# Performance work log

Measured on AMD Instinct MI355X. Metric: run time of the kernel, lower is better.

Reference implementation:

```python
import jax, jax.numpy as jnp
import numpy as np

R, H, K, C = 8, 8, 4096, 128  # residual stages, subvectors, codebook size, subvector dim
B, S = 2, 2048


def setup_inputs() -> dict:
    key = jax.random.key(0)
    k1, k2 = jax.random.split(key)
    x = jax.random.normal(k1, (B, S, H * C), dtype=jnp.float32)
    codebook = jax.random.normal(k2, (R, H, K, C), dtype=jnp.float32) * 0.1
    return {"x": x, "codebook": codebook}


def _encode(x, codebook):
    b, s, f = x.shape
    # x.view(b,s,8,2,64).transpose(3,4).flatten(2)  -> interleave the two 64-dim halves per head
    xp = x.reshape(b, s, 8, 2, 64).transpose(0, 1, 2, 4, 3).reshape(b, s, f)
    prescale = jnp.linalg.norm(xp, axis=-1, keepdims=True)  # (b,s,1)
    xn = xp / prescale
    # (b s) h c  -> permute to (h, N, c)
    t0 = xn.reshape(b * s, H, C).transpose(1, 0, 2)  # (H, N, C)

    def step(t, cb_r):
        # cb_r: (H, K, C). Squared-euclidean argmin == torch.cdist argmin (sqrt is monotone,
        # and the ||t||^2 term is constant over k so it is dropped).
        d = jnp.sum(cb_r * cb_r, axis=-1)[:, None, :] - 2.0 * jnp.einsum('hnc,hkc->hnk', t, cb_r)
        idx = jnp.argmin(d, axis=-1)  # (H, N)
        q = jnp.take_along_axis(cb_r, idx[..., None], axis=1)  # (H, N, C)
        return t - q, idx.astype(jnp.int32)

    _, codes = jax.lax.scan(step, t0, codebook)  # codes: (R, H, N)
    return codes, prescale


def _decode(codes, prescale, codebook):
    # gather codebook entries: (R, H, N, C)
    g = jnp.take_along_axis(codebook, codes[..., None], axis=2)
    n = codes.shape[2]
    # permute(0,2,1,3).flatten(-2).sum(0): (R,N,H*C) summed over residual stages
    rec = g.transpose(0, 2, 1, 3).reshape(R, n, H * C).sum(0)  # (N, H*C)
    b = prescale.shape[0]
    return rec.reshape(b, -1, H * C) * prescale


def reference(x, codebook):
    codes, prescale = _encode(x, codebook)
    return _decode(codes, prescale, codebook)
```

## Files before the change

### kernel.cpp

```cpp
#include <hip/hip_runtime.h>

#define R_STAGES 8
#define H_HEADS  8
#define K_CODES  4096
#define C_DIM    128
#define N_TOK    4096
#define FEAT     1024
#define HKC      (H_HEADS * K_CODES * C_DIM)

#define MARGIN   1.2e-2f
#define WCAP     512
#define TMS      260

typedef _Float16 half8  __attribute__((ext_vector_type(8)));
typedef _Float16 half4v __attribute__((ext_vector_type(4)));
typedef float    f32x4  __attribute__((ext_vector_type(4)));

#define MFMA16(A, B, C) __builtin_amdgcn_mfma_f32_16x16x32_f16((A), (B), (C), 0, 0, 0)


__global__ void kc_prep(const float* __restrict__ x, float* __restrict__ t,
                        float* __restrict__ ps) {
    int n = blockIdx.x;
    const float* xr = x + (size_t)n * FEAT;

    double ss = 0.0;
    for (int i = threadIdx.x; i < FEAT; i += 256) {
        float v = xr[i];
        ss += (double)v * (double)v;
    }
    for (int off = 32; off > 0; off >>= 1) ss += __shfl_down(ss, off);

    __shared__ double sred[4];
    __shared__ float s_p;
    int wid = threadIdx.x >> 6, lane = threadIdx.x & 63;
    if (lane == 0) sred[wid] = ss;
    __syncthreads();
    if (threadIdx.x == 0) {
        double tot = sred[0] + sred[1] + sred[2] + sred[3];
        float p = (float)sqrt(tot);
        ps[n] = p;
        s_p = p;
    }
    __syncthreads();
    float p = s_p;

    for (int i = threadIdx.x; i < FEAT; i += 256) {
        int c = i & 127;
        float v = xr[(i & ~127) + ((c & 1) << 6) + (c >> 1)];
        size_t o = ((size_t)(i >> 7) * N_TOK + n) * C_DIM + c;
        t[o] = v / p;
    }
}

__global__ void kc_cvtn(const float* __restrict__ cb, _Float16* __restrict__ cb16,
                        float* __restrict__ cn) {
    int w = (blockIdx.x << 2) + (threadIdx.x >> 6);
    int lane = threadIdx.x & 63;
    const float* row = cb + (size_t)w * C_DIM;
    float a = row[lane], b = row[lane + 64];
    _Float16* dr = cb16 + (size_t)w * C_DIM;
    dr[lane]      = (_Float16)a;
    dr[lane + 64] = (_Float16)b;
    double s = (double)a * a + (double)b * b;
    for (int off = 32; off > 0; off >>= 1) s += __shfl_down(s, off);
    if (lane == 0) cn[w] = (float)s;
}

__device__ __forceinline__ void stage_body(
    const float* __restrict__ cbh32, const _Float16* __restrict__ cbh16,
    const float* __restrict__ cnh, float* __restrict__ th) {

    __shared__ _Float16 tmin[64 * TMS];
    __shared__ float    rbs[256][4];
    __shared__ float    mtok[64];
    __shared__ int      wl[WCAP];
    __shared__ double   eD[WCAP];
    __shared__ int      eI[WCAP];
    __shared__ int      winner[64];
    __shared__ int      wlCnt;

    const int tid  = threadIdx.x;
    const int w    = tid >> 6;
    const int lane = tid & 63;
    const int col  = lane & 15;
    const int rblk = lane >> 4;

    if (tid == 0) wlCnt = 0;

    half8 tf[4][4];
#pragma unroll
    for (int g = 0; g < 4; ++g) {
        const float* trow = th + (size_t)(g * 16 + col) * C_DIM;
#pragma unroll
        for (int j = 0; j < 4; ++j) {
            const float* p = trow + j * 32 + rblk * 8;
            f32x4 lo = *(const f32x4*)p;
            f32x4 hi = *(const f32x4*)(p + 4);
            half8 v;
            v[0] = (_Float16)lo[0]; v[1] = (_Float16)lo[1];
            v[2] = (_Float16)lo[2]; v[3] = (_Float16)lo[3];
            v[4] = (_Float16)hi[0]; v[5] = (_Float16)hi[1];
            v[6] = (_Float16)hi[2]; v[7] = (_Float16)hi[3];
            tf[g][j] = v;
        }
    }

    const int kbase = w << 10;
    const _Float16* cbA = cbh16 + (size_t)(kbase + col) * C_DIM + rblk * 8;
    const float*    cnA = cnh + kbase + (rblk << 2);

    auto loadA = [&](int it, half8* A, f32x4& cv) {
        const _Float16* p = cbA + (size_t)it * (16 * C_DIM);
#pragma unroll
        for (int j = 0; j < 4; ++j) A[j] = *(const half8*)(p + j * 32);
        cv = *(const f32x4*)(cnA + it * 16);
    };

    float rbg0 = 3.4e38f, rbg1 = 3.4e38f, rbg2 = 3.4e38f, rbg3 = 3.4e38f;

    auto screen = [&](const half8* A, const f32x4& cv, int wtile) {
        f32x4 a0 = {0.f,0.f,0.f,0.f}, a1 = {0.f,0.f,0.f,0.f};
        f32x4 a2 = {0.f,0.f,0.f,0.f}, a3 = {0.f,0.f,0.f,0.f};
#pragma unroll
        for (int j = 0; j < 4; ++j) {
            a0 = MFMA16(A[j], tf[0][j], a0);
            a1 = MFMA16(A[j], tf[1][j], a1);
            a2 = MFMA16(A[j], tf[2][j], a2);
            a3 = MFMA16(A[j], tf[3][j], a3);
        }
        float m0 = fminf(fminf(cv[0] - 2.f*a0[0], cv[1] - 2.f*a0[1]),
                         fminf(cv[2] - 2.f*a0[2], cv[3] - 2.f*a0[3]));
        float m1 = fminf(fminf(cv[0] - 2.f*a1[0], cv[1] - 2.f*a1[1]),
                         fminf(cv[2] - 2.f*a1[2], cv[3] - 2.f*a1[3]));
        float m2 = fminf(fminf(cv[0] - 2.f*a2[0], cv[1] - 2.f*a2[1]),
                         fminf(cv[2] - 2.f*a2[2], cv[3] - 2.f*a2[3]));
        float m3 = fminf(fminf(cv[0] - 2.f*a3[0], cv[1] - 2.f*a3[1]),
                         fminf(cv[2] - 2.f*a3[2], cv[3] - 2.f*a3[3]));
        m0 = fminf(m0, __shfl_xor(m0, 16)); m0 = fminf(m0, __shfl_xor(m0, 32));
        m1 = fminf(m1, __shfl_xor(m1, 16)); m1 = fminf(m1, __shfl_xor(m1, 32));
        m2 = fminf(m2, __shfl_xor(m2, 16)); m2 = fminf(m2, __shfl_xor(m2, 32));
        m3 = fminf(m3, __shfl_xor(m3, 16)); m3 = fminf(m3, __shfl_xor(m3, 32));
        rbg0 = fminf(rbg0, m0); rbg1 = fminf(rbg1, m1);
        rbg2 = fminf(rbg2, m2); rbg3 = fminf(rbg3, m3);
        if (rblk == 0) {
            tmin[(col)      * TMS + wtile] = (_Float16)m0;
            tmin[(16 + col) * TMS + wtile] = (_Float16)m1;
            tmin[(32 + col) * TMS + wtile] = (_Float16)m2;
            tmin[(48 + col) * TMS + wtile] = (_Float16)m3;
        }
    };

    {
        half8 A0[4], A1[4], A2[4], A3[4];
        f32x4 v0, v1, v2, v3;
        loadA(0, A0, v0); loadA(1, A1, v1); loadA(2, A2, v2); loadA(3, A3, v3);
        const int wbase = w << 6;
#pragma unroll 1
        for (int j = 0; j < 16; ++j) {
            const int b4 = j << 2;
            screen(A0, v0, wbase + b4);
            if (j < 15) loadA(b4 + 4, A0, v0);
            screen(A1, v1, wbase + b4 + 1);
            if (j < 15) loadA(b4 + 5, A1, v1);
            screen(A2, v2, wbase + b4 + 2);
            if (j < 15) loadA(b4 + 6, A2, v2);
            screen(A3, v3, wbase + b4 + 3);
            if (j < 15) loadA(b4 + 7, A3, v3);
        }
    }
    rbs[tid][0] = rbg0; rbs[tid][1] = rbg1; rbs[tid][2] = rbg2; rbs[tid][3] = rbg3;
    __syncthreads();

    if (tid < 64) {
        const int g = tid >> 4, c2 = tid & 15;
        float m = 3.4e38f;
#pragma unroll
        for (int ww = 0; ww < 4; ++ww) m = fminf(m, rbs[ww * 64 + c2][g]);
        mtok[tid] = m;
    }
    __syncthreads();

    {
        const int tok = tid >> 2, q = tid & 3;
        const float thr = mtok[tok] + MARGIN;
        const half4v* rowp = (const half4v*)(tmin + tok * TMS + (q << 6));
#pragma unroll 4
        for (int j4 = 0; j4 < 16; ++j4) {
            half4v v = rowp[j4];
#pragma unroll
            for (int e = 0; e < 4; ++e) {
                if ((float)v[e] < thr) {
                    int idx = atomicAdd(&wlCnt, 1);
                    if (idx < WCAP) wl[idx] = (tok << 8) | ((q << 6) + (j4 << 2) + e);
                }
            }
        }
    }
    __syncthreads();

    int E = wlCnt;
    if (E <= WCAP) {
        for (int e0 = 0; e0 < E; e0 += 16) {
            const int e = e0 + (tid >> 4);
            double bd = 1e300; int bi = 0x7fffffff;
            if (e < E) {
                const int meta = wl[e];
                const int tok = meta >> 8;
                const int k = ((meta & 255) << 4) + (tid & 15);
                const float* crow = cbh32 + (size_t)k * C_DIM;
                const float* trw  = th + (size_t)tok * C_DIM;
                double cx0=0,cx1=0,cx2=0,cx3=0,d0=0,d1=0,d2=0,d3=0;
#pragma unroll 4
                for (int c = 0; c < C_DIM; c += 4) {
                    double cv0 = crow[c],   tv0 = trw[c];
                    double cv1 = crow[c+1], tv1 = trw[c+1];
                    double cv2 = crow[c+2], tv2 = trw[c+2];
                    double cv3 = crow[c+3], tv3 = trw[c+3];
                    cx0 = fma(cv0,cv0,cx0); d0 = fma(tv0,cv0,d0);
                    cx1 = fma(cv1,cv1,cx1); d1 = fma(tv1,cv1,d1);
                    cx2 = fma(cv2,cv2,cx2); d2 = fma(tv2,cv2,d2);
                    cx3 = fma(cv3,cv3,cx3); d3 = fma(tv3,cv3,d3);
                }
                bd = ((cx0+cx1)+(cx2+cx3)) - 2.0*((d0+d1)+(d2+d3));
                bi = k;
            }
#pragma unroll
            for (int off = 1; off < 16; off <<= 1) {
                double od = __shfl_xor(bd, off);
                int    oi = __shfl_xor(bi, off);
                if (od < bd || (od == bd && oi < bi)) { bd = od; bi = oi; }
            }
            if ((tid & 15) == 0 && e < E) { eD[e >> 0] = bd; eI[e] = bi; }
        }
        __syncthreads();
        if (tid < 64) {
            double bd = 1e300; int bi = 0x7fffffff;
            for (int e = 0; e < E; ++e) {
                if ((wl[e] >> 8) == tid) {
                    double d = eD[e]; int i2 = eI[e];
                    if (d < bd || (d == bd && i2 < bi)) { bd = d; bi = i2; }
                }
            }
            winner[tid] = bi;
        }
        __syncthreads();
    } else {
        for (int ot = 0; ot < 64; ++ot) {
            const float* trw = th + (size_t)ot * C_DIM;
            double bd = 1e300; int bi = 0x7fffffff;
            for (int k = tid; k < K_CODES; k += 256) {
                const float* crow = cbh32 + (size_t)k * C_DIM;
                double cx0=0,cx1=0,cx2=0,cx3=0,d0=0,d1=0,d2=0,d3=0;
                for (int c = 0; c < C_DIM; c += 4) {
                    double cv0 = crow[c],   tv0 = trw[c];
                    double cv1 = crow[c+1], tv1 = trw[c+1];
                    double cv2 = crow[c+2], tv2 = trw[c+2];
                    double cv3 = crow[c+3], tv3 = trw[c+3];
                    cx0 = fma(cv0,cv0,cx0); d0 = fma(tv0,cv0,d0);
                    cx1 = fma(cv1,cv1,cx1); d1 = fma(tv1,cv1,d1);
                    cx2 = fma(cv2,cv2,cx2); d2 = fma(tv2,cv2,d2);
                    cx3 = fma(cv3,cv3,cx3); d3 = fma(tv3,cv3,d3);
                }
                double d = ((cx0+cx1)+(cx2+cx3)) - 2.0*((d0+d1)+(d2+d3));
                if (d < bd || (d == bd && k < bi)) { bd = d; bi = k; }
            }
            for (int off = 1; off <= 32; off <<= 1) {
                double od = __shfl_xor(bd, off);
                int    oi = __shfl_xor(bi, off);
                if (od < bd || (od == bd && oi < bi)) { bd = od; bi = oi; }
            }
            if (lane == 0) { eD[w] = bd; eI[w] = bi; }
            __syncthreads();
            if (tid == 0) {
                double b2 = eD[0]; int i2 = eI[0];
                for (int q = 1; q < 4; ++q) {
                    if (eD[q] < b2 || (eD[q] == b2 && eI[q] < i2)) { b2 = eD[q]; i2 = eI[q]; }
                }
                winner[ot] = i2;
            }
            __syncthreads();
        }
    }

    for (int i = tid; i < 64 * C_DIM; i += 256) {
        const int tok = i >> 7, c = i & 127;
        th[(size_t)tok * C_DIM + c] -= cbh32[(size_t)winner[tok] * C_DIM + c];
    }
    __syncthreads();
}

__global__ __launch_bounds__(256, 2)
void kc_all(const float* __restrict__ cb32, const _Float16* __restrict__ cb16,
            const float* __restrict__ cn, float* __restrict__ t) {
    const int h  = blockIdx.x & 7;
    const int n0 = (blockIdx.x >> 3) << 6;
    float* th = t + ((size_t)h * N_TOK + n0) * C_DIM;
#pragma unroll 1
    for (int r = 0; r < R_STAGES; ++r) {
        const size_t off = (size_t)(r * H_HEADS + h) * K_CODES;
        stage_body(cb32 + off * C_DIM, cb16 + off * C_DIM, cn + off, th);
    }
}

__global__ __launch_bounds__(256, 2)
void kc_stage_one(const float* __restrict__ cb32, const _Float16* __restrict__ cb16,
                  const float* __restrict__ cn, float* __restrict__ t) {
    const int h  = blockIdx.x & 7;
    const int n0 = (blockIdx.x >> 3) << 6;
    float* th = t + ((size_t)h * N_TOK + n0) * C_DIM;
    const size_t off = (size_t)h * K_CODES;
    stage_body(cb32 + off * C_DIM, cb16 + off * C_DIM, cn + off, th);
}

__global__ void kc_out(const float* __restrict__ x, const float* __restrict__ t,
                       const float* __restrict__ ps, float* __restrict__ out) {
    int n = blockIdx.x;
    float p = ps[n];
    const float* xr = x + (size_t)n * FEAT;
    for (int i = threadIdx.x; i < FEAT; i += 256) {
        int c = i & 127;
        float v = xr[(i & ~127) + ((c & 1) << 6) + (c >> 1)];
        float t0 = v / p;
        float tf = t[((size_t)(i >> 7) * N_TOK + n) * C_DIM + c];
        out[(size_t)n * FEAT + i] = (t0 - tf) * p;
    }
}

extern "C" void kernel_launch(void* const* d_in, const int* in_sizes, int n_in,
                              void* d_out, int out_size, void* d_ws, size_t ws_size,
                              hipStream_t stream) {
    const float* x  = (const float*)d_in[0];
    const float* cb = (const float*)d_in[1];
    float* out = (float*)d_out;

    float*    t    = (float*)d_ws;
    float*    ps   = (float*)((char*)d_ws + 16777216);
    float*    cn   = (float*)((char*)d_ws + 16793600);
    _Float16* cb16 = (_Float16*)((char*)d_ws + 17842176);

    const bool full = (ws_size >= 84951040ull);

    kc_prep<<<N_TOK, 256, 0, stream>>>(x, t, ps);

    if (full) {
        kc_cvtn<<<(R_STAGES * H_HEADS * K_CODES) / 4, 256, 0, stream>>>(cb, cb16, cn);
        kc_all<<<H_HEADS * (N_TOK / 64), 256, 0, stream>>>(cb, cb16, cn, t);
    } else {
        for (int r = 0; r < R_STAGES; ++r) {
            kc_cvtn<<<(H_HEADS * K_CODES) / 4, 256, 0, stream>>>(
                cb + (size_t)r * HKC, cb16, cn + (size_t)r * H_HEADS * K_CODES);
            kc_stage_one<<<H_HEADS * (N_TOK / 64), 256, 0, stream>>>(
                cb + (size_t)r * HKC, cb16, cn + (size_t)r * H_HEADS * K_CODES, t);
        }
    }

    kc_out<<<N_TOK, 256, 0, stream>>>(x, t, ps, out);
}
```

Measured before the change: 1.063 ms.

## Double block to 512 threads splitting codebook screen across eight waves

The stage kernel now runs with 512 threads (8 waves) per block. Each wave screens 512 codes instead of 1024, and the prefetch depth drops from four tiles to two to save registers. The per-tile min reductions are packed as half2 pairs so one shuffle serves two token groups. The refinement and update loops are re-strided for the larger block. The aim is more parallelism per block and lower latency per stage, at the cost of more register and LDS pressure and half-precision running minima in the screen.

New measurement: 1.583 ms. +49.0%, slower.

```diff
diff --git a/kernel.cpp b/kernel.cpp
--- a/kernel.cpp
+++ b/kernel.cpp
@@ -14,9 +14,21 @@
 
 typedef _Float16 half8  __attribute__((ext_vector_type(8)));
 typedef _Float16 half4v __attribute__((ext_vector_type(4)));
+typedef _Float16 half2v __attribute__((ext_vector_type(2)));
 typedef float    f32x4  __attribute__((ext_vector_type(4)));
 
 #define MFMA16(A, B, C) __builtin_amdgcn_mfma_f32_16x16x32_f16((A), (B), (C), 0, 0, 0)
+
+union H2U { half2v h; int i; };
+__device__ __forceinline__ half2v hmin2(half2v a, half2v b) {
+    half2v r;
+    r[0] = a[0] < b[0] ? a[0] : b[0];
+    r[1] = a[1] < b[1] ? a[1] : b[1];
+    return r;
+}
+__device__ __forceinline__ half2v shfl_xor_h2(half2v v, int m) {
+    H2U u; u.h = v; u.i = __shfl_xor(u.i, m); return u.h;
+}
 
 
 __global__ void kc_prep(const float* __restrict__ x, float* __restrict__ t,
@@ -72,7 +84,7 @@
     const float* __restrict__ cnh, float* __restrict__ th) {
 
     __shared__ _Float16 tmin[64 * TMS];
-    __shared__ float    rbs[256][4];
+    __shared__ float    rbs[512][5];
     __shared__ float    mtok[64];
     __shared__ int      wl[WCAP];
     __shared__ double   eD[WCAP];
@@ -106,7 +118,7 @@
         }
     }
 
-    const int kbase = w << 10;
+    const int kbase = w << 9;
     const _Float16* cbA = cbh16 + (size_t)(kbase + col) * C_DIM + rblk * 8;
     const float*    cnA = cnh + kbase + (rblk << 2);
 
@@ -117,7 +129,8 @@
         cv = *(const f32x4*)(cnA + it * 16);
     };
 
-    float rbg0 = 3.4e38f, rbg1 = 3.4e38f, rbg2 = 3.4e38f, rbg3 = 3.4e38f;
+    half2v rb01, rb23;
+    rb01[0] = rb01[1] = rb23[0] = rb23[1] = (_Float16)60000.0f;
 
     auto screen = [&](const half8* A, const f32x4& cv, int wtile) {
         f32x4 a0 = {0.f,0.f,0.f,0.f}, a1 = {0.f,0.f,0.f,0.f};
@@ -137,62 +150,62 @@
                          fminf(cv[2] - 2.f*a2[2], cv[3] - 2.f*a2[3]));
         float m3 = fminf(fminf(cv[0] - 2.f*a3[0], cv[1] - 2.f*a3[1]),
                          fminf(cv[2] - 2.f*a3[2], cv[3] - 2.f*a3[3]));
-        m0 = fminf(m0, __shfl_xor(m0, 16)); m0 = fminf(m0, __shfl_xor(m0, 32));
-        m1 = fminf(m1, __shfl_xor(m1, 16)); m1 = fminf(m1, __shfl_xor(m1, 32));
-        m2 = fminf(m2, __shfl_xor(m2, 16)); m2 = fminf(m2, __shfl_xor(m2, 32));
-        m3 = fminf(m3, __shfl_xor(m3, 16)); m3 = fminf(m3, __shfl_xor(m3, 32));
-        rbg0 = fminf(rbg0, m0); rbg1 = fminf(rbg1, m1);
-        rbg2 = fminf(rbg2, m2); rbg3 = fminf(rbg3, m3);
+        half2v p01, p23;
+        p01[0] = (_Float16)m0; p01[1] = (_Float16)m1;
+        p23[0] = (_Float16)m2; p23[1] = (_Float16)m3;
+        p01 = hmin2(p01, shfl_xor_h2(p01, 16));
+        p23 = hmin2(p23, shfl_xor_h2(p23, 16));
+        p01 = hmin2(p01, shfl_xor_h2(p01, 32));
+        p23 = hmin2(p23, shfl_xor_h2(p23, 32));
+        rb01 = hmin2(rb01, p01);
+        rb23 = hmin2(rb23, p23);
         if (rblk == 0) {
-            tmin[(col)      * TMS + wtile] = (_Float16)m0;
-            tmin[(16 + col) * TMS + wtile] = (_Float16)m1;
-            tmin[(32 + col) * TMS + wtile] = (_Float16)m2;
-            tmin[(48 + col) * TMS + wtile] = (_Float16)m3;
+            tmin[(col)      * TMS + wtile] = p01[0];
+            tmin[(16 + col) * TMS + wtile] = p01[1];
+            tmin[(32 + col) * TMS + wtile] = p23[0];
+            tmin[(48 + col) * TMS + wtile] = p23[1];
         }
     };
 
     {
-        half8 A0[4], A1[4], A2[4], A3[4];
-        f32x4 v0, v1, v2, v3;
-        loadA(0, A0, v0); loadA(1, A1, v1); loadA(2, A2, v2); loadA(3, A3, v3);
-        const int wbase = w << 6;
+        half8 A0[4], A1[4];
+        f32x4 v0, v1;
+        loadA(0, A0, v0); loadA(1, A1, v1);
+        const int wbase = w << 5;
 #pragma unroll 1
         for (int j = 0; j < 16; ++j) {
-            const int b4 = j << 2;
-            screen(A0, v0, wbase + b4);
-            if (j < 15) loadA(b4 + 4, A0, v0);
-            screen(A1, v1, wbase + b4 + 1);
-            if (j < 15) loadA(b4 + 5, A1, v1);
-            screen(A2, v2, wbase + b4 + 2);
-            if (j < 15) loadA(b4 + 6, A2, v2);
-            screen(A3, v3, wbase + b4 + 3);
-            if (j < 15) loadA(b4 + 7, A3, v3);
-        }
-    }
-    rbs[tid][0] = rbg0; rbs[tid][1] = rbg1; rbs[tid][2] = rbg2; rbs[tid][3] = rbg3;
+            const int b2 = j << 1;
+            screen(A0, v0, wbase + b2);
+            if (j < 15) loadA(b2 + 2, A0, v0);
+            screen(A1, v1, wbase + b2 + 1);
+            if (j < 15) loadA(b2 + 3, A1, v1);
+        }
+    }
+    rbs[tid][0] = (float)rb01[0]; rbs[tid][1] = (float)rb01[1];
+    rbs[tid][2] = (float)rb23[0]; rbs[tid][3] = (float)rb23[1];
     __syncthreads();
 
     if (tid < 64) {
         const int g = tid >> 4, c2 = tid & 15;
         float m = 3.4e38f;
 #pragma unroll
-        for (int ww = 0; ww < 4; ++ww) m = fminf(m, rbs[ww * 64 + c2][g]);
+        for (int ww = 0; ww < 8; ++ww) m = fminf(m, rbs[(ww << 6) + c2][g]);
         mtok[tid] = m;
     }
     __syncthreads();
 
     {
-        const int tok = tid >> 2, q = tid & 3;
+        const int tok = tid >> 3, q = tid & 7;
         const float thr = mtok[tok] + MARGIN;
-        const half4v* rowp = (const half4v*)(tmin + tok * TMS + (q << 6));
-#pragma unroll 4
-        for (int j4 = 0; j4 < 16; ++j4) {
+        const half4v* rowp = (const half4v*)(tmin + tok * TMS + (q << 5));
+#pragma unroll 2
+        for (int j4 = 0; j4 < 8; ++j4) {
             half4v v = rowp[j4];
 #pragma unroll
             for (int e = 0; e < 4; ++e) {
                 if ((float)v[e] < thr) {
                     int idx = atomicAdd(&wlCnt, 1);
-                    if (idx < WCAP) wl[idx] = (tok << 8) | ((q << 6) + (j4 << 2) + e);
+                    if (idx < WCAP) wl[idx] = (tok << 8) | ((q << 5) + (j4 << 2) + e);
                 }
             }
         }
@@ -201,7 +214,7 @@
 
     int E = wlCnt;
     if (E <= WCAP) {
-        for (int e0 = 0; e0 < E; e0 += 16) {
+        for (int e0 = 0; e0 < E; e0 += 32) {
             const int e = e0 + (tid >> 4);
             double bd = 1e300; int bi = 0x7fffffff;
             if (e < E) {
@@ -231,7 +244,7 @@
                 int    oi = __shfl_xor(bi, off);
                 if (od < bd || (od == bd && oi < bi)) { bd = od; bi = oi; }
             }
-            if ((tid & 15) == 0 && e < E) { eD[e >> 0] = bd; eI[e] = bi; }
+            if ((tid & 15) == 0 && e < E) { eD[e] = bd; eI[e] = bi; }
         }
         __syncthreads();
         if (tid < 64) {
@@ -249,7 +262,7 @@
         for (int ot = 0; ot < 64; ++ot) {
             const float* trw = th + (size_t)ot * C_DIM;
             double bd = 1e300; int bi = 0x7fffffff;
-            for (int k = tid; k < K_CODES; k += 256) {
+            for (int k = tid; k < K_CODES; k += 512) {
                 const float* crow = cbh32 + (size_t)k * C_DIM;
                 double cx0=0,cx1=0,cx2=0,cx3=0,d0=0,d1=0,d2=0,d3=0;
                 for (int c = 0; c < C_DIM; c += 4) {
@@ -274,7 +287,7 @@
             __syncthreads();
             if (tid == 0) {
                 double b2 = eD[0]; int i2 = eI[0];
-                for (int q = 1; q < 4; ++q) {
+                for (int q = 1; q < 8; ++q) {
                     if (eD[q] < b2 || (eD[q] == b2 && eI[q] < i2)) { b2 = eD[q]; i2 = eI[q]; }
                 }
                 winner[ot] = i2;
@@ -283,14 +296,14 @@
         }
     }
 
-    for (int i = tid; i < 64 * C_DIM; i += 256) {
+    for (int i = tid; i < 64 * C_DIM; i += 512) {
         const int tok = i >> 7, c = i & 127;
         th[(size_t)tok * C_DIM + c] -= cbh32[(size_t)winner[tok] * C_DIM + c];
     }
     __syncthreads();
 }
 
-__global__ __launch_bounds__(256, 2)
+__global__ __launch_bounds__(512, 4)
 void kc_all(const float* __restrict__ cb32, const _Float16* __restrict__ cb16,
             const float* __restrict__ cn, float* __restrict__ t) {
     const int h  = blockIdx.x & 7;
@@ -303,7 +316,7 @@
     }
 }
 
-__global__ __launch_bounds__(256, 2)
+__global__ __launch_bounds__(512, 4)
 void kc_stage_one(const float* __restrict__ cb32, const _Float16* __restrict__ cb16,
                   const float* __restrict__ cn, float* __restrict__ t) {
     const int h  = blockIdx.x & 7;
@@ -345,12 +358,12 @@
 
     if (full) {
         kc_cvtn<<<(R_STAGES * H_HEADS * K_CODES) / 4, 256, 0, stream>>>(cb, cb16, cn);
-        kc_all<<<H_HEADS * (N_TOK / 64), 256, 0, stream>>>(cb, cb16, cn, t);
+        kc_all<<<H_HEADS * (N_TOK / 64), 512, 0, stream>>>(cb, cb16, cn, t);
     } else {
         for (int r = 0; r < R_STAGES; ++r) {
             kc_cvtn<<<(H_HEADS * K_CODES) / 4, 256, 0, stream>>>(
                 cb + (size_t)r * HKC, cb16, cn + (size_t)r * H_HEADS * K_CODES);
-            kc_stage_one<<<H_HEADS * (N_TOK / 64), 256, 0, stream>>>(
+            kc_stage_one<<<H_HEADS * (N_TOK / 64), 512, 0, stream>>>(
                 cb + (size_t)r * HKC, cb16, cn + (size_t)r * H_HEADS * K_CODES, t);
         }
     }
```
